# Kernel optimization log

Measured on AMD Instinct MI355X. Metric: run time of the kernel, lower is better.

## Reference

```python
import jax, jax.numpy as jnp
import numpy as np

N_NODES = 100000
IN_F = 512
HID = 256
HEADS = 1
CLASSES = 40
ALPHA = 0.5
EPS = 1e-5


def layer_norm(x, g, b):
    mu = jnp.mean(x, axis=-1, keepdims=True)
    var = jnp.mean(jnp.square(x - mu), axis=-1, keepdims=True)
    return g * (x - mu) / jnp.sqrt(var + EPS) + b


def full_attention_conv(qs, ks, vs):
    # qs, ks, vs: [N, H, D]; global (Frobenius) L2 normalization as in torch.norm(p=2)
    qs = qs / jnp.linalg.norm(qs.reshape(-1))
    ks = ks / jnp.linalg.norm(ks.reshape(-1))
    N = qs.shape[0]
    kvs = jnp.einsum('lhm,lhd->hmd', ks, vs)                  # [H, D, D]
    attention_num = jnp.einsum('nhm,hmd->nhd', qs, kvs) + N * vs
    ks_sum = jnp.sum(ks, axis=0)                              # [H, D]
    attention_normalizer = jnp.einsum('nhm,hm->nh', qs, ks_sum)[..., None] + N
    return attention_num / attention_normalizer               # [N, H, D]


def trans_layer(h, prev, Wq, bq, Wk, bk, Wv, bv, ln_g, ln_b):
    N = h.shape[0]
    q = (h @ Wq + bq).reshape(N, HEADS, HID)
    k = (h @ Wk + bk).reshape(N, HEADS, HID)
    v = (h @ Wv + bv).reshape(N, HEADS, HID)
    attn = full_attention_conv(q, k, v).mean(axis=1)          # [N, HID]
    h = ALPHA * attn + (1.0 - ALPHA) * prev
    return layer_norm(h, ln_g, ln_b)


def setup_inputs() -> dict:
    key = jax.random.key(0)
    ks = jax.random.split(key, 16)
    s_in = 1.0 / np.sqrt(IN_F)
    s_h = 1.0 / np.sqrt(HID)
    d = {
        'x': jax.random.normal(ks[0], (N_NODES, IN_F), jnp.float32),
        'edge_index': jax.random.randint(ks[1], (2, 1600000), 0, N_NODES, jnp.int64),
        'W_in': jax.random.normal(ks[2], (IN_F, HID), jnp.float32) * s_in,
        'b_in': jnp.zeros((HID,), jnp.float32),
        'ln0_g': jnp.ones((HID,), jnp.float32),
        'ln0_b': jnp.zeros((HID,), jnp.float32),
        'Wq0': jax.random.normal(ks[3], (HID, HID * HEADS), jnp.float32) * s_h,
        'bq0': jnp.zeros((HID * HEADS,), jnp.float32),
        'Wk0': jax.random.normal(ks[4], (HID, HID * HEADS), jnp.float32) * s_h,
        'bk0': jnp.zeros((HID * HEADS,), jnp.float32),
        'Wv0': jax.random.normal(ks[5], (HID, HID * HEADS), jnp.float32) * s_h,
        'bv0': jnp.zeros((HID * HEADS,), jnp.float32),
        'ln1_g': jnp.ones((HID,), jnp.float32),
        'ln1_b': jnp.zeros((HID,), jnp.float32),
        'Wq1': jax.random.normal(ks[6], (HID, HID * HEADS), jnp.float32) * s_h,
        'bq1': jnp.zeros((HID * HEADS,), jnp.float32),
        'Wk1': jax.random.normal(ks[7], (HID, HID * HEADS), jnp.float32) * s_h,
        'bk1': jnp.zeros((HID * HEADS,), jnp.float32),
        'Wv1': jax.random.normal(ks[8], (HID, HID * HEADS), jnp.float32) * s_h,
        'bv1': jnp.zeros((HID * HEADS,), jnp.float32),
        'ln2_g': jnp.ones((HID,), jnp.float32),
        'ln2_b': jnp.zeros((HID,), jnp.float32),
        'W_out': jax.random.normal(ks[9], (HID, CLASSES), jnp.float32) * s_h,
        'b_out': jnp.zeros((CLASSES,), jnp.float32),
    }
    return d


def reference(x, edge_index, W_in, b_in, ln0_g, ln0_b,
              Wq0, bq0, Wk0, bk0, Wv0, bv0, ln1_g, ln1_b,
              Wq1, bq1, Wk1, bk1, Wv1, bv1, ln2_g, ln2_b,
              W_out, b_out):
    # SGFormer forward with use_graph=False, eval mode (dropout no-op).
    h = jax.nn.relu(layer_norm(x @ W_in + b_in, ln0_g, ln0_b))
    prev = h
    h = trans_layer(h, prev, Wq0, bq0, Wk0, bk0, Wv0, bv0, ln1_g, ln1_b)
    prev = h
    h = trans_layer(h, prev, Wq1, bq1, Wk1, bk1, Wv1, bv1, ln2_g, ln2_b)
    return h @ W_out + b_out  # [N, CLASSES]
```

## Files before the change

kernel.cpp:

```cpp
#include <hip/hip_runtime.h>


typedef __attribute__((ext_vector_type(8))) short short8;
typedef __attribute__((ext_vector_type(4))) float floatx4;

__device__ __forceinline__ float bf2f(short u) {
    union { unsigned int i; float f; } v;
    v.i = ((unsigned int)(unsigned short)u) << 16;
    return v.f;
}
__device__ __forceinline__ short f2bf(float f) {
    union { float f; unsigned int i; } v; v.f = f;
    unsigned int b = v.i + 0x7fffu + ((v.i >> 16) & 1u);
    return (short)(b >> 16);
}

#define HID 256
#define MROWS 100000
#define EPSLN 1e-5f

__device__ __forceinline__ void stage_a256(const short* __restrict__ A, short* As,
                                           int row0, int wave, int lane)
{
    const int base = wave * 512;
#pragma unroll
    for (int it = 0; it < 8; ++it) {
        int J = base + it * 64 + lane;
        int row = J >> 5, jj = J & 31;
        int c = jj ^ (row & 31);
        int rowg = min(row0 + row, MROWS - 1);
        const short* gp = A + (size_t)rowg * HID + c * 8;
        __builtin_amdgcn_global_load_lds(
            (const __attribute__((address_space(1))) void*)gp,
            (__attribute__((address_space(3))) void*)&As[(size_t)(base + it * 64) * 8],
            16, 0, 0);
    }
}
__device__ __forceinline__ short8 read_a256(const short* As, int m, int ki, int quad, int l15)
{
    int row = m * 16 + l15;
    int phys = (ki * 4 + quad) ^ (row & 31);
    return *(const short8*)&As[((size_t)row * 32 + phys) * 8];
}

__global__ __launch_bounds__(256, 3)
void qkv_kernel(const short* __restrict__ h,
                const short* __restrict__ BTq, const short* __restrict__ BTk,
                const short* __restrict__ BTv,
                const float* __restrict__ bq, const float* __restrict__ bk,
                const float* __restrict__ bv,
                short* __restrict__ qO, short* __restrict__ kO, short* __restrict__ vO,
                float* __restrict__ sqq, float* __restrict__ sqk,
                float* __restrict__ ksum)
{
    __shared__ short As[64 * 256];
    __shared__ short Cb[16 * 264];
    __shared__ float scr;

    const int tid = threadIdx.x, wave = tid >> 6, lane = tid & 63;
    const int quad = lane >> 4, l15 = lane & 15;
    const int row0 = blockIdx.x * 64, nb = wave * 64;

    stage_a256(h, As, row0, wave, lane);
    __syncthreads();

    const short* BTs[3] = {BTq, BTk, BTv};
    short* Cs[3] = {qO, kO, vO};
    const float* bs[3] = {bq, bk, bv};

#pragma unroll
    for (int out = 0; out < 3; ++out) {
        const short* BT = BTs[out];
        short* C = Cs[out];
        const float* bias = bs[out];

        floatx4 acc[4][4];
#pragma unroll
        for (int m = 0; m < 4; m++)
#pragma unroll
            for (int n = 0; n < 4; n++) acc[m][n] = (floatx4)0.0f;

#pragma unroll
        for (int ki = 0; ki < 8; ++ki) {
            short8 a[4];
#pragma unroll
            for (int m = 0; m < 4; ++m) a[m] = read_a256(As, m, ki, quad, l15);
#pragma unroll
            for (int n = 0; n < 4; ++n) {
                short8 b = *(const short8*)(BT + (size_t)(nb + n * 16 + l15) * 256 + ki * 32 + quad * 8);
#pragma unroll
                for (int m = 0; m < 4; ++m)
                    acc[m][n] = __builtin_amdgcn_mfma_f32_16x16x32_bf16(a[m], b, acc[m][n], 0, 0, 0);
            }
        }

        float bn[4];
#pragma unroll
        for (int n = 0; n < 4; n++) bn[n] = bias[nb + n * 16 + l15];

        float ssq = 0.f;
        float csum[4] = {0.f, 0.f, 0.f, 0.f};
#pragma unroll
        for (int m = 0; m < 4; m++)
#pragma unroll
            for (int r = 0; r < 4; r++) {
                int rl = m * 16 + quad * 4 + r;
                bool valid = (row0 + rl) < MROWS;
#pragma unroll
                for (int n = 0; n < 4; n++) {
                    float val = acc[m][n][r] + bn[n];
                    acc[m][n][r] = val;
                    if (valid) {
                        if (out < 2) ssq += val * val;
                        if (out == 1) csum[n] += val;
                    }
                }
            }
        if (out < 2) {
#pragma unroll
            for (int off = 32; off; off >>= 1) ssq += __shfl_down(ssq, off);
            if (tid == 0) scr = 0.f;
            __syncthreads();
            if (lane == 0) atomicAdd(&scr, ssq);
            __syncthreads();
            if (tid == 0) atomicAdd(out == 0 ? sqq : sqk, scr);
        }
        if (out == 1) {
#pragma unroll
            for (int n = 0; n < 4; n++) {
                float cv = csum[n];
                cv += __shfl_xor(cv, 16);
                cv += __shfl_xor(cv, 32);
                if (quad == 0) atomicAdd(&ksum[nb + n * 16 + l15], cv);
            }
        }
#pragma unroll
        for (int m = 0; m < 4; ++m) {
            __syncthreads();
#pragma unroll
            for (int n = 0; n < 4; ++n)
#pragma unroll
                for (int r = 0; r < 4; ++r)
                    Cb[(quad * 4 + r) * 264 + nb + n * 16 + l15] = f2bf(acc[m][n][r]);
            __syncthreads();
#pragma unroll
            for (int ch = tid; ch < 512; ch += 256) {
                int rl = ch >> 5, co = (ch & 31) * 8;
                int row = row0 + m * 16 + rl;
                if (row < MROWS)
                    *(short8*)(C + (size_t)row * 256 + co) = *(const short8*)&Cb[rl * 264 + co];
            }
        }
    }
}

__global__ __launch_bounds__(256, 3)
void attn_kernel(const short* __restrict__ q, const short* __restrict__ KVt,
                 const short* __restrict__ v, short* __restrict__ h,
                 const float* __restrict__ lng, const float* __restrict__ lnb,
                 float Nf)
{
    __shared__ short As[64 * 256];
    __shared__ short Cb[16 * 264];
    __shared__ float redS[64][4], redQ[64][4];
    __shared__ float rowm[64], rowr[64], denA[64];

    const int tid = threadIdx.x, wave = tid >> 6, lane = tid & 63;
    const int quad = lane >> 4, l15 = lane & 15;
    const int row0 = blockIdx.x * 64, nb = wave * 64;

    stage_a256(q, As, row0, wave, lane);
    __syncthreads();

    floatx4 acc[4][4];
#pragma unroll
    for (int m = 0; m < 4; m++)
#pragma unroll
        for (int n = 0; n < 4; n++) acc[m][n] = (floatx4)0.0f;
    floatx4 accd[4];
#pragma unroll
    for (int m = 0; m < 4; m++) accd[m] = (floatx4)0.0f;

#pragma unroll
    for (int ki = 0; ki < 8; ++ki) {
        short8 a[4];
#pragma unroll
        for (int m = 0; m < 4; ++m) a[m] = read_a256(As, m, ki, quad, l15);
#pragma unroll
        for (int n = 0; n < 4; ++n) {
            short8 b = *(const short8*)(KVt + (size_t)(nb + n * 16 + l15) * 256 + ki * 32 + quad * 8);
#pragma unroll
            for (int m = 0; m < 4; ++m)
                acc[m][n] = __builtin_amdgcn_mfma_f32_16x16x32_bf16(a[m], b, acc[m][n], 0, 0, 0);
        }
        if (wave == 0) {
            short8 bd = *(const short8*)(KVt + (size_t)(256 + l15) * 256 + ki * 32 + quad * 8);
#pragma unroll
            for (int m = 0; m < 4; ++m)
                accd[m] = __builtin_amdgcn_mfma_f32_16x16x32_bf16(a[m], bd, accd[m], 0, 0, 0);
        }
    }
    if (wave == 0 && l15 == 0) {
#pragma unroll
        for (int m = 0; m < 4; m++)
#pragma unroll
            for (int r = 0; r < 4; r++)
                denA[m * 16 + quad * 4 + r] = accd[m][r];
    }
    __syncthreads();

#pragma unroll
    for (int m = 0; m < 4; m++)
#pragma unroll
        for (int r = 0; r < 4; r++) {
            int rl = m * 16 + quad * 4 + r;
            int rowc = min(row0 + rl, MROWS - 1);
            float rden = 1.0f / (denA[rl] + Nf);
            float s = 0.f, s2 = 0.f;
#pragma unroll
            for (int n = 0; n < 4; n++) {
                int col = nb + n * 16 + l15;
                float vv = bf2f(v[(size_t)rowc * 256 + col]);
                float pv = bf2f(h[(size_t)rowc * 256 + col]);
                float val = 0.5f * (acc[m][n][r] + Nf * vv) * rden + 0.5f * pv;
                acc[m][n][r] = val;
                s += val; s2 += val * val;
            }
#pragma unroll
            for (int off = 1; off < 16; off <<= 1) {
                s += __shfl_xor(s, off);
                s2 += __shfl_xor(s2, off);
            }
            if (l15 == 0) { redS[rl][wave] = s; redQ[rl][wave] = s2; }
        }
    __syncthreads();
    if (tid < 64) {
        float s = redS[tid][0] + redS[tid][1] + redS[tid][2] + redS[tid][3];
        float s2 = redQ[tid][0] + redQ[tid][1] + redQ[tid][2] + redQ[tid][3];
        float mean = s * (1.0f / 256.0f);
        float var = s2 * (1.0f / 256.0f) - mean * mean;
        rowm[tid] = mean;
        rowr[tid] = rsqrtf(var + EPSLN);
    }
    __syncthreads();
    float g[4], bb[4];
#pragma unroll
    for (int n = 0; n < 4; n++) {
        g[n] = lng[nb + n * 16 + l15];
        bb[n] = lnb[nb + n * 16 + l15];
    }
#pragma unroll
    for (int m = 0; m < 4; ++m) {
        __syncthreads();
#pragma unroll
        for (int n = 0; n < 4; ++n)
#pragma unroll
            for (int r = 0; r < 4; ++r) {
                int rl = m * 16 + quad * 4 + r;
                float x = (acc[m][n][r] - rowm[rl]) * rowr[rl] * g[n] + bb[n];
                Cb[(quad * 4 + r) * 264 + nb + n * 16 + l15] = f2bf(x);
            }
        __syncthreads();
#pragma unroll
        for (int ch = tid; ch < 512; ch += 256) {
            int rl = ch >> 5, co = (ch & 31) * 8;
            int row = row0 + m * 16 + rl;
            if (row < MROWS)
                *(short8*)(h + (size_t)row * 256 + co) = *(const short8*)&Cb[rl * 264 + co];
        }
    }
}

__global__ __launch_bounds__(256, 3)
void in_kernel(const float* __restrict__ x, const short* __restrict__ WinT,
               const float* __restrict__ b_in, const float* __restrict__ lng,
               const float* __restrict__ lnb, short* __restrict__ h)
{
    __shared__ short As[64 * 128];
    __shared__ short Cb[16 * 264];
    __shared__ float redS[64][4], redQ[64][4];
    __shared__ float rowm[64], rowr[64];

    const int tid = threadIdx.x, wave = tid >> 6, lane = tid & 63;
    const int quad = lane >> 4, l15 = lane & 15;
    const int row0 = blockIdx.x * 64, nb = wave * 64;

    floatx4 acc[4][4];
#pragma unroll
    for (int m = 0; m < 4; m++)
#pragma unroll
        for (int n = 0; n < 4; n++) acc[m][n] = (floatx4)0.0f;

    for (int slab = 0; slab < 512; slab += 128) {
        __syncthreads();
#pragma unroll
        for (int it = 0; it < 4; ++it) {
            int J = it * 256 + tid;
            int row = J >> 4, jj = J & 15, c = jj ^ (row & 15);
            int rowg = min(row0 + row, MROWS - 1);
            const float* gp = x + (size_t)rowg * 512 + slab + c * 8;
            floatx4 x0 = *(const floatx4*)gp;
            floatx4 x1 = *(const floatx4*)(gp + 4);
            short8 s8;
#pragma unroll
            for (int i = 0; i < 4; ++i) { s8[i] = f2bf(x0[i]); s8[i + 4] = f2bf(x1[i]); }
            *(short8*)&As[(size_t)J * 8] = s8;
        }
        __syncthreads();
#pragma unroll
        for (int ki = 0; ki < 4; ++ki) {
            short8 a[4];
#pragma unroll
            for (int m = 0; m < 4; ++m) {
                int row = m * 16 + l15;
                int phys = (ki * 4 + quad) ^ (row & 15);
                a[m] = *(const short8*)&As[((size_t)row * 16 + phys) * 8];
            }
#pragma unroll
            for (int n = 0; n < 4; ++n) {
                short8 b = *(const short8*)(WinT + (size_t)(nb + n * 16 + l15) * 512 + slab + ki * 32 + quad * 8);
#pragma unroll
                for (int m = 0; m < 4; ++m)
                    acc[m][n] = __builtin_amdgcn_mfma_f32_16x16x32_bf16(a[m], b, acc[m][n], 0, 0, 0);
            }
        }
    }
    float bn[4];
#pragma unroll
    for (int n = 0; n < 4; n++) bn[n] = b_in[nb + n * 16 + l15];
#pragma unroll
    for (int m = 0; m < 4; m++)
#pragma unroll
        for (int r = 0; r < 4; r++) {
            int rl = m * 16 + quad * 4 + r;
            float s = 0.f, s2 = 0.f;
#pragma unroll
            for (int n = 0; n < 4; n++) {
                float val = acc[m][n][r] + bn[n];
                acc[m][n][r] = val;
                s += val; s2 += val * val;
            }
#pragma unroll
            for (int off = 1; off < 16; off <<= 1) {
                s += __shfl_xor(s, off);
                s2 += __shfl_xor(s2, off);
            }
            if (l15 == 0) { redS[rl][wave] = s; redQ[rl][wave] = s2; }
        }
    __syncthreads();
    if (tid < 64) {
        float s = redS[tid][0] + redS[tid][1] + redS[tid][2] + redS[tid][3];
        float s2 = redQ[tid][0] + redQ[tid][1] + redQ[tid][2] + redQ[tid][3];
        float mean = s * (1.0f / 256.0f);
        float var = s2 * (1.0f / 256.0f) - mean * mean;
        rowm[tid] = mean;
        rowr[tid] = rsqrtf(var + EPSLN);
    }
    __syncthreads();
    float g[4], bb[4];
#pragma unroll
    for (int n = 0; n < 4; n++) {
        g[n] = lng[nb + n * 16 + l15];
        bb[n] = lnb[nb + n * 16 + l15];
    }
#pragma unroll
    for (int m = 0; m < 4; ++m) {
        __syncthreads();
#pragma unroll
        for (int n = 0; n < 4; ++n)
#pragma unroll
            for (int r = 0; r < 4; ++r) {
                int rl = m * 16 + quad * 4 + r;
                float xv = (acc[m][n][r] - rowm[rl]) * rowr[rl] * g[n] + bb[n];
                Cb[(quad * 4 + r) * 264 + nb + n * 16 + l15] = f2bf(fmaxf(xv, 0.f));
            }
        __syncthreads();
#pragma unroll
        for (int ch = tid; ch < 512; ch += 256) {
            int rl = ch >> 5, co = (ch & 31) * 8;
            int row = row0 + m * 16 + rl;
            if (row < MROWS)
                *(short8*)(h + (size_t)row * 256 + co) = *(const short8*)&Cb[rl * 264 + co];
        }
    }
}

__global__ __launch_bounds__(256)
void kv_kernel(const short* __restrict__ k, const short* __restrict__ v,
               float* __restrict__ KV, int M)
{
    __shared__ short ksT[128][40];
    __shared__ short vsT[128][40];
    const int t = threadIdx.x, wave = t >> 6, lane = t & 63;
    const int quad = lane >> 4, l15 = lane & 15;
    const int mb = blockIdx.x * 128, nbb = blockIdx.y * 128;
    const int chunk = (M + (int)gridDim.z - 1) / (int)gridDim.z;
    const int rbeg = blockIdx.z * chunk;
    const int rend = min(M, rbeg + chunk);

    floatx4 acc[2][8];
#pragma unroll
    for (int m = 0; m < 2; m++)
#pragma unroll
        for (int j = 0; j < 8; j++) acc[m][j] = (floatx4)0.0f;

    const int lr = t >> 3, c0 = (t & 7) * 16;
    const int wm = wave * 32;

    for (int r0 = rbeg; r0 < rend; r0 += 32) {
        int gr = r0 + lr;
        short8 k0 = (short8)(short)0, k1 = (short8)(short)0;
        short8 v0 = (short8)(short)0, v1 = (short8)(short)0;
        if (gr < rend) {
            const short* kp = k + (size_t)gr * HID + mb + c0;
            const short* vp = v + (size_t)gr * HID + nbb + c0;
            k0 = *(const short8*)kp;  k1 = *(const short8*)(kp + 8);
            v0 = *(const short8*)vp;  v1 = *(const short8*)(vp + 8);
        }
        __syncthreads();
#pragma unroll
        for (int i = 0; i < 8; i++) {
            ksT[c0 + i][lr] = k0[i];  ksT[c0 + 8 + i][lr] = k1[i];
            vsT[c0 + i][lr] = v0[i];  vsT[c0 + 8 + i][lr] = v1[i];
        }
        __syncthreads();
        short8 a0 = *(const short8*)&ksT[wm + l15][quad * 8];
        short8 a1 = *(const short8*)&ksT[wm + 16 + l15][quad * 8];
#pragma unroll
        for (int j = 0; j < 8; j++) {
            short8 b = *(const short8*)&vsT[j * 16 + l15][quad * 8];
            acc[0][j] = __builtin_amdgcn_mfma_f32_16x16x32_bf16(a0, b, acc[0][j], 0, 0, 0);
            acc[1][j] = __builtin_amdgcn_mfma_f32_16x16x32_bf16(a1, b, acc[1][j], 0, 0, 0);
        }
    }
#pragma unroll
    for (int mi = 0; mi < 2; mi++)
#pragma unroll
        for (int j = 0; j < 8; j++)
#pragma unroll
            for (int r = 0; r < 4; r++) {
                int m = mb + wm + mi * 16 + quad * 4 + r;
                int n = nbb + j * 16 + l15;
                atomicAdd(&KV[(size_t)m * HID + n], acc[mi][j][r]);
            }
}

__global__ void scale_kernel(const float* __restrict__ KV, const float* __restrict__ ksum,
                             const float* __restrict__ sq, short* __restrict__ KVt)
{
    float s = rsqrtf(sq[0]) * rsqrtf(sq[1]);
    int d = blockIdx.x;
    int m = threadIdx.x;
    float val;
    if (d < 256)       val = KV[(size_t)m * HID + d] * s;
    else if (d == 256) val = ksum[m] * s;
    else               val = 0.f;
    KVt[(size_t)d * HID + m] = f2bf(val);
}

__global__ __launch_bounds__(256)
void gemm_out(const short* __restrict__ A, const short* __restrict__ BT,
              const float* __restrict__ bias, float* __restrict__ Out, int M)
{
    const int tid = threadIdx.x, wave = tid >> 6, lane = tid & 63;
    const int quad = lane >> 4, l15 = lane & 15;
    const int row0 = blockIdx.x * 128 + wave * 32;
    const int K = 256;
    floatx4 acc[2][3];
#pragma unroll
    for (int m = 0; m < 2; m++)
#pragma unroll
        for (int n = 0; n < 3; n++) acc[m][n] = (floatx4)0.0f;

    int ra0 = min(row0 + l15, M - 1);
    int ra1 = min(row0 + 16 + l15, M - 1);
    for (int kk = 0; kk < K; kk += 32) {
        short8 a0 = *(const short8*)(A + (size_t)ra0 * K + kk + quad * 8);
        short8 a1 = *(const short8*)(A + (size_t)ra1 * K + kk + quad * 8);
#pragma unroll
        for (int n = 0; n < 3; n++) {
            int col = n * 16 + l15;
            short8 b = (short8)(short)0;
            if (col < 40) b = *(const short8*)(BT + (size_t)col * K + kk + quad * 8);
            acc[0][n] = __builtin_amdgcn_mfma_f32_16x16x32_bf16(a0, b, acc[0][n], 0, 0, 0);
            acc[1][n] = __builtin_amdgcn_mfma_f32_16x16x32_bf16(a1, b, acc[1][n], 0, 0, 0);
        }
    }
#pragma unroll
    for (int m = 0; m < 2; m++)
#pragma unroll
        for (int n = 0; n < 3; n++)
#pragma unroll
            for (int r = 0; r < 4; r++) {
                int row = row0 + m * 16 + quad * 4 + r;
                int col = n * 16 + l15;
                if (row < M && col < 40)
                    Out[(size_t)row * 40 + col] = acc[m][n][r] + bias[col];
            }
}

struct TJobs { const float* src[8]; short* dst[8]; int R[8]; int C[8]; };

__global__ void wtrans(TJobs j)
{
    int job = blockIdx.y;
    int R = j.R[job], Cc = j.C[job];
    const float* s = j.src[job];
    short* d = j.dst[job];
    int n = R * Cc;
    for (int idx = blockIdx.x * 256 + threadIdx.x; idx < n; idx += gridDim.x * 256) {
        int r = idx / Cc, c = idx - r * Cc;
        d[(size_t)c * R + r] = f2bf(s[idx]);
    }
}

__global__ void zerof(float* p, int n)
{
    int i = blockIdx.x * 256 + threadIdx.x;
    if (i < n) p[i] = 0.f;
}

extern "C" void kernel_launch(void* const* d_in, const int* in_sizes, int n_in,
                              void* d_out, int out_size, void* d_ws, size_t ws_size,
                              hipStream_t stream)
{
    const float* x    = (const float*)d_in[0];
    const float* W_in = (const float*)d_in[2];
    const float* b_in = (const float*)d_in[3];
    const float* ln0g = (const float*)d_in[4];
    const float* ln0b = (const float*)d_in[5];
    const float* Wq0  = (const float*)d_in[6];  const float* bq0 = (const float*)d_in[7];
    const float* Wk0  = (const float*)d_in[8];  const float* bk0 = (const float*)d_in[9];
    const float* Wv0  = (const float*)d_in[10]; const float* bv0 = (const float*)d_in[11];
    const float* ln1g = (const float*)d_in[12]; const float* ln1b = (const float*)d_in[13];
    const float* Wq1  = (const float*)d_in[14]; const float* bq1 = (const float*)d_in[15];
    const float* Wk1  = (const float*)d_in[16]; const float* bk1 = (const float*)d_in[17];
    const float* Wv1  = (const float*)d_in[18]; const float* bv1 = (const float*)d_in[19];
    const float* ln2g = (const float*)d_in[20]; const float* ln2b = (const float*)d_in[21];
    const float* W_out = (const float*)d_in[22]; const float* b_out = (const float*)d_in[23];

    const int M = MROWS;
    char* ws = (char*)d_ws;
    size_t off = 0;
    auto alloc = [&](size_t bytes) -> char* {
        char* p = ws + off;
        off += (bytes + 255) & ~(size_t)255;
        return p;
    };
    short* h = (short*)alloc((size_t)M * HID * 2);
    short* q = (short*)alloc((size_t)M * HID * 2);
    short* k = (short*)alloc((size_t)M * HID * 2);
    short* v = (short*)alloc((size_t)M * HID * 2);
    short* WinT  = (short*)alloc((size_t)512 * 256 * 2);
    short* WqT0  = (short*)alloc((size_t)65536 * 2);
    short* WkT0  = (short*)alloc((size_t)65536 * 2);
    short* WvT0  = (short*)alloc((size_t)65536 * 2);
    short* WqT1  = (short*)alloc((size_t)65536 * 2);
    short* WkT1  = (short*)alloc((size_t)65536 * 2);
    short* WvT1  = (short*)alloc((size_t)65536 * 2);
    short* WoutT = (short*)alloc((size_t)40 * 256 * 2);
    float* zbase = (float*)alloc((size_t)(65536 * 2 + 256 * 2 + 4) * 4);
    float* KV0 = zbase;
    float* KV1 = zbase + 65536;
    float* ksum0 = zbase + 131072;
    float* ksum1 = ksum0 + 256;
    float* sq = ksum1 + 256;
    short* KVt0 = (short*)alloc((size_t)272 * 256 * 2);
    short* KVt1 = (short*)alloc((size_t)272 * 256 * 2);

    const int ZN = 65536 * 2 + 256 * 2 + 4;
    zerof<<<dim3((ZN + 255) / 256), 256, 0, stream>>>(zbase, ZN);

    TJobs tj;
    tj.src[0] = W_in;  tj.dst[0] = WinT;  tj.R[0] = 512; tj.C[0] = 256;
    tj.src[1] = Wq0;   tj.dst[1] = WqT0;  tj.R[1] = 256; tj.C[1] = 256;
    tj.src[2] = Wk0;   tj.dst[2] = WkT0;  tj.R[2] = 256; tj.C[2] = 256;
    tj.src[3] = Wv0;   tj.dst[3] = WvT0;  tj.R[3] = 256; tj.C[3] = 256;
    tj.src[4] = Wq1;   tj.dst[4] = WqT1;  tj.R[4] = 256; tj.C[4] = 256;
    tj.src[5] = Wk1;   tj.dst[5] = WkT1;  tj.R[5] = 256; tj.C[5] = 256;
    tj.src[6] = Wv1;   tj.dst[6] = WvT1;  tj.R[6] = 256; tj.C[6] = 256;
    tj.src[7] = W_out; tj.dst[7] = WoutT; tj.R[7] = 256; tj.C[7] = 40;
    wtrans<<<dim3(512, 8), 256, 0, stream>>>(tj);

    const int GB = (M + 63) / 64;
    const float Nf = (float)M;

    in_kernel<<<GB, 256, 0, stream>>>(x, WinT, b_in, ln0g, ln0b, h);
    qkv_kernel<<<GB, 256, 0, stream>>>(h, WqT0, WkT0, WvT0, bq0, bk0, bv0,
                                       q, k, v, sq + 0, sq + 1, ksum0);
    kv_kernel<<<dim3(2, 2, 256), 256, 0, stream>>>(k, v, KV0, M);
    scale_kernel<<<272, 256, 0, stream>>>(KV0, ksum0, sq + 0, KVt0);
    attn_kernel<<<GB, 256, 0, stream>>>(q, KVt0, v, h, ln1g, ln1b, Nf);
    qkv_kernel<<<GB, 256, 0, stream>>>(h, WqT1, WkT1, WvT1, bq1, bk1, bv1,
                                       q, k, v, sq + 2, sq + 3, ksum1);
    kv_kernel<<<dim3(2, 2, 256), 256, 0, stream>>>(k, v, KV1, M);
    scale_kernel<<<272, 256, 0, stream>>>(KV1, ksum1, sq + 2, KVt1);
    attn_kernel<<<GB, 256, 0, stream>>>(q, KVt1, v, h, ln2g, ln2b, Nf);
    gemm_out<<<(M + 127) / 128, 256, 0, stream>>>(h, WoutT, b_out, (float*)d_out, M);
}
```

Before: 1.062 ms.

## Prefetch next slab/row tiles in input and KV kernels; stage epilogue loads via LDS

The input-projection kernel now double-buffers its LDS tile and issues the next slab's global loads into registers before the current slab's MFMAs, so memory latency overlaps compute. The KV-reduction kernel prefetches the next row's k/v vectors while running MFMAs on the current tile. The attention epilogue now stages the v and h rows into LDS with coalesced direct-to-LDS loads instead of scattered per-element global reads. These add LDS use and register pressure, which may reduce occupancy.

```diff
diff --git a/kernel.cpp b/kernel.cpp
--- a/kernel.cpp
+++ b/kernel.cpp
@@ -36,6 +36,22 @@
             16, 0, 0);
     }
 }
+__device__ __forceinline__ void stage_lin256(const short* __restrict__ A, short* As,
+                                             int row0, int wave, int lane)
+{
+    const int base = wave * 512;
+#pragma unroll
+    for (int it = 0; it < 8; ++it) {
+        int J = base + it * 64 + lane;
+        int row = J >> 5, jj = J & 31;
+        int rowg = min(row0 + row, MROWS - 1);
+        const short* gp = A + (size_t)rowg * HID + jj * 8;
+        __builtin_amdgcn_global_load_lds(
+            (const __attribute__((address_space(1))) void*)gp,
+            (__attribute__((address_space(3))) void*)&As[(size_t)(base + it * 64) * 8],
+            16, 0, 0);
+    }
+}
 __device__ __forceinline__ short8 read_a256(const short* As, int m, int ki, int quad, int l15)
 {
     int row = m * 16 + l15;
@@ -209,20 +225,36 @@
     }
     __syncthreads();
 
+    stage_lin256(v, As, row0, wave, lane);
+    __syncthreads();
 #pragma unroll
     for (int m = 0; m < 4; m++)
 #pragma unroll
         for (int r = 0; r < 4; r++) {
             int rl = m * 16 + quad * 4 + r;
-            int rowc = min(row0 + rl, MROWS - 1);
             float rden = 1.0f / (denA[rl] + Nf);
-            float s = 0.f, s2 = 0.f;
 #pragma unroll
             for (int n = 0; n < 4; n++) {
                 int col = nb + n * 16 + l15;
-                float vv = bf2f(v[(size_t)rowc * 256 + col]);
-                float pv = bf2f(h[(size_t)rowc * 256 + col]);
-                float val = 0.5f * (acc[m][n][r] + Nf * vv) * rden + 0.5f * pv;
+                float vv = bf2f(As[(size_t)rl * 256 + col]);
+                acc[m][n][r] = 0.5f * (acc[m][n][r] + Nf * vv) * rden;
+            }
+        }
+    __syncthreads();
+
+    stage_lin256(h, As, row0, wave, lane);
+    __syncthreads();
+#pragma unroll
+    for (int m = 0; m < 4; m++)
+#pragma unroll
+        for (int r = 0; r < 4; r++) {
+            int rl = m * 16 + quad * 4 + r;
+            float s = 0.f, s2 = 0.f;
+#pragma unroll
+            for (int n = 0; n < 4; n++) {
+                int col = nb + n * 16 + l15;
+                float pv = bf2f(As[(size_t)rl * 256 + col]);
+                float val = acc[m][n][r] + 0.5f * pv;
                 acc[m][n][r] = val;
                 s += val; s2 += val * val;
             }
@@ -276,7 +308,7 @@
                const float* __restrict__ b_in, const float* __restrict__ lng,
                const float* __restrict__ lnb, short* __restrict__ h)
 {
-    __shared__ short As[64 * 128];
+    __shared__ short As[2][64 * 128];
     __shared__ short Cb[16 * 264];
     __shared__ float redS[64][4], redQ[64][4];
     __shared__ float rowm[64], rowr[64];
@@ -291,22 +323,37 @@
 #pragma unroll
         for (int n = 0; n < 4; n++) acc[m][n] = (floatx4)0.0f;
 
-    for (int slab = 0; slab < 512; slab += 128) {
-        __syncthreads();
+    floatx4 xr[4][2];
+    auto issue = [&](int slab) {
 #pragma unroll
         for (int it = 0; it < 4; ++it) {
             int J = it * 256 + tid;
             int row = J >> 4, jj = J & 15, c = jj ^ (row & 15);
             int rowg = min(row0 + row, MROWS - 1);
             const float* gp = x + (size_t)rowg * 512 + slab + c * 8;
-            floatx4 x0 = *(const floatx4*)gp;
-            floatx4 x1 = *(const floatx4*)(gp + 4);
+            xr[it][0] = *(const floatx4*)gp;
+            xr[it][1] = *(const floatx4*)(gp + 4);
+        }
+    };
+    auto commit = [&](short* dst) {
+#pragma unroll
+        for (int it = 0; it < 4; ++it) {
+            int J = it * 256 + tid;
             short8 s8;
 #pragma unroll
-            for (int i = 0; i < 4; ++i) { s8[i] = f2bf(x0[i]); s8[i + 4] = f2bf(x1[i]); }
-            *(short8*)&As[(size_t)J * 8] = s8;
-        }
-        __syncthreads();
+            for (int i = 0; i < 4; ++i) { s8[i] = f2bf(xr[it][0][i]); s8[i + 4] = f2bf(xr[it][1][i]); }
+            *(short8*)&dst[(size_t)J * 8] = s8;
+        }
+    };
+
+    issue(0);
+    commit(As[0]);
+    __syncthreads();
+
+#pragma unroll
+    for (int s = 0; s < 4; ++s) {
+        if (s < 3) issue((s + 1) * 128);
+        const short* cur = As[s & 1];
 #pragma unroll
         for (int ki = 0; ki < 4; ++ki) {
             short8 a[4];
@@ -314,15 +361,19 @@
             for (int m = 0; m < 4; ++m) {
                 int row = m * 16 + l15;
                 int phys = (ki * 4 + quad) ^ (row & 15);
-                a[m] = *(const short8*)&As[((size_t)row * 16 + phys) * 8];
+                a[m] = *(const short8*)&cur[((size_t)row * 16 + phys) * 8];
             }
 #pragma unroll
             for (int n = 0; n < 4; ++n) {
-                short8 b = *(const short8*)(WinT + (size_t)(nb + n * 16 + l15) * 512 + slab + ki * 32 + quad * 8);
+                short8 b = *(const short8*)(WinT + (size_t)(nb + n * 16 + l15) * 512 + s * 128 + ki * 32 + quad * 8);
 #pragma unroll
                 for (int m = 0; m < 4; ++m)
                     acc[m][n] = __builtin_amdgcn_mfma_f32_16x16x32_bf16(a[m], b, acc[m][n], 0, 0, 0);
             }
+        }
+        if (s < 3) {
+            commit(As[(s + 1) & 1]);
+            __syncthreads();
         }
     }
     float bn[4];
@@ -407,16 +458,19 @@
     const int lr = t >> 3, c0 = (t & 7) * 16;
     const int wm = wave * 32;
 
-    for (int r0 = rbeg; r0 < rend; r0 += 32) {
-        int gr = r0 + lr;
-        short8 k0 = (short8)(short)0, k1 = (short8)(short)0;
-        short8 v0 = (short8)(short)0, v1 = (short8)(short)0;
+    short8 k0, k1, v0, v1;
+    auto loadrow = [&](int gr, short8& a0, short8& a1, short8& b0, short8& b1) {
+        a0 = a1 = b0 = b1 = (short8)(short)0;
         if (gr < rend) {
             const short* kp = k + (size_t)gr * HID + mb + c0;
             const short* vp = v + (size_t)gr * HID + nbb + c0;
-            k0 = *(const short8*)kp;  k1 = *(const short8*)(kp + 8);
-            v0 = *(const short8*)vp;  v1 = *(const short8*)(vp + 8);
-        }
+            a0 = *(const short8*)kp;  a1 = *(const short8*)(kp + 8);
+            b0 = *(const short8*)vp;  b1 = *(const short8*)(vp + 8);
+        }
+    };
+    loadrow(rbeg + lr, k0, k1, v0, v1);
+
+    for (int r0 = rbeg; r0 < rend; r0 += 32) {
         __syncthreads();
 #pragma unroll
         for (int i = 0; i < 8; i++) {
@@ -424,6 +478,9 @@
             vsT[c0 + i][lr] = v0[i];  vsT[c0 + 8 + i][lr] = v1[i];
         }
         __syncthreads();
+        bool more = (r0 + 32) < rend;
+        short8 nk0, nk1, nv0, nv1;
+        if (more) loadrow(r0 + 32 + lr, nk0, nk1, nv0, nv1);
         short8 a0 = *(const short8*)&ksT[wm + l15][quad * 8];
         short8 a1 = *(const short8*)&ksT[wm + 16 + l15][quad * 8];
 #pragma unroll
@@ -432,6 +489,7 @@
             acc[0][j] = __builtin_amdgcn_mfma_f32_16x16x32_bf16(a0, b, acc[0][j], 0, 0, 0);
             acc[1][j] = __builtin_amdgcn_mfma_f32_16x16x32_bf16(a1, b, acc[1][j], 0, 0, 0);
         }
+        if (more) { k0 = nk0; k1 = nk1; v0 = nv0; v1 = nv1; }
     }
 #pragma unroll
     for (int mi = 0; mi < 2; mi++)
```

Result: no change. 1.058 ms (-0.4%).
